# Kernel tuning notes

Hardware: AMD Instinct MI355X
Metric: run time of the kernel (lower is better)

Reference implementation:

```python
import jax, jax.numpy as jnp
import numpy as np

NUM_EXPERTS = 64
TOP_K = 8
HIDDEN = 2048
MLP = 768
TOKENS = 1024


def setup_inputs() -> dict:
    key = jax.random.key(0)
    ks = jax.random.split(key, 5)
    hidden_states = jax.random.normal(ks[0], (TOKENS, HIDDEN), dtype=jnp.float32)
    # lecun-normal-ish scaling (std = 1/sqrt(fan_in))
    router_w = jax.random.normal(ks[1], (HIDDEN, NUM_EXPERTS), dtype=jnp.float32) / np.sqrt(HIDDEN)
    gate_proj = jax.random.normal(ks[2], (NUM_EXPERTS, HIDDEN, MLP), dtype=jnp.float32) / np.sqrt(HIDDEN)
    up_proj = jax.random.normal(ks[3], (NUM_EXPERTS, HIDDEN, MLP), dtype=jnp.float32) / np.sqrt(HIDDEN)
    down_proj = jax.random.normal(ks[4], (NUM_EXPERTS, MLP, HIDDEN), dtype=jnp.float32) / np.sqrt(MLP)
    return {
        "hidden_states": hidden_states,
        "router_w": router_w,
        "gate_proj": gate_proj,
        "up_proj": up_proj,
        "down_proj": down_proj,
    }


def reference(hidden_states, router_w, gate_proj, up_proj, down_proj):
    # Router: [T, E]
    router_logits = hidden_states @ router_w
    # Top-k routing, softmax renormalized over the selected k (norm_topk_prob=True)
    routing_weights, selected_experts = jax.lax.top_k(router_logits, k=TOP_K)
    routing_weights = jax.nn.softmax(routing_weights, axis=-1)  # [T, k]

    sel_flat = selected_experts.ravel()  # [T*k] int32
    # Duplicate each token for each of its k experts: [T*k, H]
    x_exp = jnp.repeat(hidden_states, TOP_K, axis=0)

    # prepare_routing: sort token copies by expert id, count per-expert group sizes
    sort_idx = jnp.argsort(sel_flat)          # stable sort of expert ids
    x_sorted = x_exp[sort_idx]                # [T*k, H] grouped by expert
    group_sizes = jnp.zeros((NUM_EXPERTS,), dtype=jnp.int32).at[sel_flat].add(1)
    unsort_idx = jnp.argsort(sort_idx)

    # Grouped GEMMs (megablox-style) via ragged_dot
    gate_out = jax.lax.ragged_dot(x_sorted, gate_proj, group_sizes)   # [T*k, M]
    up_out = jax.lax.ragged_dot(x_sorted, up_proj, group_sizes)       # [T*k, M]
    down_out = jax.lax.ragged_dot(jax.nn.silu(gate_out) * up_out, down_proj, group_sizes)  # [T*k, H]

    # Unsort back to (token, k) order and combine with routing weights
    unsorted = down_out[unsort_idx].reshape(-1, TOP_K, HIDDEN)
    return jnp.sum(unsorted * routing_weights[..., None], axis=1)  # [T, H]
```

## Files before the change

### kernel.cpp

```cpp
#include <hip/hip_runtime.h>
#include <hip/hip_bf16.h>

#define T_TOKENS 1024
#define HID      2048
#define NEXP     64
#define TOPK     8
#define MLP      768
#define NPAIR    (T_TOKENS * TOPK)

typedef __bf16 bf16x8 __attribute__((ext_vector_type(8)));
typedef float  f32x4  __attribute__((ext_vector_type(4)));
typedef unsigned int u32x2 __attribute__((ext_vector_type(2)));
typedef unsigned int u32x4 __attribute__((ext_vector_type(4)));

#define LDK 40

static __device__ __forceinline__ unsigned short f2bf(float f) {
    __hip_bfloat16 h = __float2bfloat16(f);
    unsigned short u;
    __builtin_memcpy(&u, &h, sizeof(u));
    return u;
}
static __device__ __forceinline__ unsigned int pk2bf(float a, float b) {
    return (unsigned int)f2bf(a) | ((unsigned int)f2bf(b) << 16);
}

__global__ __launch_bounds__(256) void router_topk_kernel(
    const float* __restrict__ hs, const float* __restrict__ rw,
    int* __restrict__ sel, float* __restrict__ wts, unsigned short* __restrict__ xb)
{
    const int lane = threadIdx.x & 63;
    const int tg   = threadIdx.x >> 6;
    const int t    = blockIdx.x * 4 + tg;

    {
        const float* xr = hs + (size_t)t * HID;
        unsigned short* xw = xb + (size_t)t * HID;
        #pragma unroll
        for (int c = 0; c < 4; ++c) {
            int i = (lane + c * 64) * 8;
            f32x4 a = *(const f32x4*)(xr + i);
            f32x4 b = *(const f32x4*)(xr + i + 4);
            u32x4 v;
            v[0] = pk2bf(a[0], a[1]); v[1] = pk2bf(a[2], a[3]);
            v[2] = pk2bf(b[0], b[1]); v[3] = pk2bf(b[2], b[3]);
            *(u32x4*)(xw + i) = v;
        }
    }

    const float4* x4 = (const float4*)(hs + (size_t)t * HID);
    float acc = 0.f;
    for (int h4 = 0; h4 < HID / 4; ++h4) {
        float4 xv = x4[h4];
        int hb = h4 * 4 * NEXP + lane;
        acc += xv.x * rw[hb] + xv.y * rw[hb + NEXP]
             + xv.z * rw[hb + 2 * NEXP] + xv.w * rw[hb + 3 * NEXP];
    }

    float v = acc;
    float tv[TOPK]; int ti[TOPK];
    for (int i = 0; i < TOPK; ++i) {
        float m = v; int mi = lane;
        for (int off = 32; off > 0; off >>= 1) {
            float om  = __shfl_xor(m, off, 64);
            int   omi = __shfl_xor(mi, off, 64);
            if (om > m || (om == m && omi < mi)) { m = om; mi = omi; }
        }
        tv[i] = m; ti[i] = mi;
        if (lane == mi) v = -__builtin_inff();
    }
    if (lane == 0) {
        float mx = tv[0], s = 0.f, e[TOPK];
        for (int i = 0; i < TOPK; ++i) { e[i] = __expf(tv[i] - mx); s += e[i]; }
        float inv = 1.f / s;
        for (int i = 0; i < TOPK; ++i) {
            wts[t * TOPK + i] = e[i] * inv;
            sel[t * TOPK + i] = ti[i];
        }
    }
}

__global__ __launch_bounds__(1024) void route_kernel(
    const int* __restrict__ sel, int* __restrict__ offsets, int* __restrict__ rows)
{
    __shared__ int cnt[NEXP];
    __shared__ int cur[NEXP];
    const int t = threadIdx.x;
    if (t < NEXP) cnt[t] = 0;
    __syncthreads();
    int e[8];
    const int p0 = t * 8;
    #pragma unroll
    for (int j = 0; j < 8; ++j) {
        e[j] = sel[p0 + j];
        atomicAdd(&cnt[e[j]], 1);
    }
    __syncthreads();
    if (t == 0) {
        int s = 0;
        for (int i = 0; i < NEXP; ++i) { cur[i] = s; offsets[i] = s; s += cnt[i]; }
        offsets[NEXP] = s;
    }
    __syncthreads();
    #pragma unroll
    for (int j = 0; j < 8; ++j) {
        int pos = atomicAdd(&cur[e[j]], 1);
        rows[pos] = p0 + j;
    }
}

__global__ __launch_bounds__(512) void gateup_kernel(
    const unsigned short* __restrict__ xb, const float* __restrict__ gw,
    const float* __restrict__ uw, const int* __restrict__ offsets,
    const int* __restrict__ rows, unsigned short* __restrict__ hb)
{
    const int bid = blockIdx.x;
    const int sw  = (bid & 7) * 96 + (bid >> 3);
    const int e   = sw / 12;
    const int n0  = (sw % 12) * 64;

    const int r0 = offsets[e];
    const int nrows = offsets[e + 1] - r0;
    if (nrows <= 0) return;

    __shared__ __align__(16) float smemf[12800];
    unsigned short* smem = (unsigned short*)smemf;

    const int thr  = threadIdx.x;
    const int wave = thr >> 6;
    const int lane = thr & 63;
    const int wg   = wave & 3;
    const int isUp = wave >> 2;
    const int fr   = lane & 15;
    const int fq   = lane >> 4;

    const int ar = thr >> 3;
    const int ac = (thr & 7) * 4;

    const int wk2 = thr & 15;
    const int wnq = (thr & 255) >> 4;
    const float* wsrc = (thr >= 256 ? uw : gw)
        + (size_t)e * HID * MLP + (size_t)(2 * wk2) * MLP + n0 + wnq * 4;
    const int mofs = (thr >= 256) ? 10240 : 7680;

    const int NS = HID / 32;

    for (int m0 = 0; m0 < nrows; m0 += 192) {
        const unsigned short *ap0, *ap1, *ap2;
        bool av0, av1, av2;
        {
            int gr0 = m0 + ar, gr1 = m0 + ar + 64, gr2 = m0 + ar + 128;
            av0 = gr0 < nrows; av1 = gr1 < nrows; av2 = gr2 < nrows;
            int p0 = av0 ? rows[r0 + gr0] : 0;
            int p1 = av1 ? rows[r0 + gr1] : 0;
            int p2 = av2 ? rows[r0 + gr2] : 0;
            ap0 = xb + (size_t)(p0 >> 3) * HID + ac;
            ap1 = xb + (size_t)(p1 >> 3) * HID + ac;
            ap2 = xb + (size_t)(p2 >> 3) * HID + ac;
        }

        u32x2 va0, va1, va2;
        f32x4 w0e, w1e, w0o, w1o;
        const u32x2 z2 = (u32x2){0u, 0u};
        const f32x4 fz = (f32x4){0.f, 0.f, 0.f, 0.f};

        auto LOAD_A = [&](int s) {
            va0 = av0 ? *(const u32x2*)(ap0 + s * 32) : z2;
            va1 = av1 ? *(const u32x2*)(ap1 + s * 32) : z2;
            va2 = av2 ? *(const u32x2*)(ap2 + s * 32) : z2;
        };
        auto WRITE_A = [&](int s) {
            unsigned short* b = smem + (s & 1) * 12800;
            *(u32x2*)(b + ar * LDK + ac) = va0;
            *(u32x2*)(b + (ar + 64) * LDK + ac) = va1;
            *(u32x2*)(b + (ar + 128) * LDK + ac) = va2;
        };
        auto LOAD_WE = [&](int s) {
            const float* wp = wsrc + (size_t)s * 32 * MLP;
            w0e = *(const f32x4*)wp;  w1e = *(const f32x4*)(wp + MLP);
        };
        auto LOAD_WO = [&](int s) {
            const float* wp = wsrc + (size_t)s * 32 * MLP;
            w0o = *(const f32x4*)wp;  w1o = *(const f32x4*)(wp + MLP);
        };
        auto WRITE_WE = [&](int s) {
            unsigned short* wb = smem + (s & 1) * 12800 + mofs;
            #pragma unroll
            for (int i = 0; i < 4; ++i)
                *(unsigned int*)(wb + (wnq * 4 + i) * LDK + 2 * wk2) = pk2bf(w0e[i], w1e[i]);
        };
        auto WRITE_WO = [&](int s) {
            unsigned short* wb = smem + (s & 1) * 12800 + mofs;
            #pragma unroll
            for (int i = 0; i < 4; ++i)
                *(unsigned int*)(wb + (wnq * 4 + i) * LDK + 2 * wk2) = pk2bf(w0o[i], w1o[i]);
        };

        f32x4 acc[3][4];
        #pragma unroll
        for (int ms = 0; ms < 3; ++ms)
            #pragma unroll
            for (int ns = 0; ns < 4; ++ns) acc[ms][ns] = fz;

        const int rem = nrows - m0 - wg * 48;

        LOAD_WE(0);
        LOAD_WO(1);
        LOAD_A(0);
        WRITE_WE(0);
        WRITE_A(0);
        LOAD_A(1);
        asm volatile("s_waitcnt lgkmcnt(0)" ::: "memory");
        __builtin_amdgcn_s_barrier();

        #define GU_MFMA(BB)                                                          \
        {                                                                            \
            const unsigned short* wbb = (BB) + mofs;                                 \
            bf16x8 aF0, aF1, aF2, wF0, wF1, wF2, wF3;                                \
            wF0 = *(const bf16x8*)(wbb + (0 * 16 + fr) * LDK + fq * 8);              \
            wF1 = *(const bf16x8*)(wbb + (1 * 16 + fr) * LDK + fq * 8);              \
            wF2 = *(const bf16x8*)(wbb + (2 * 16 + fr) * LDK + fq * 8);              \
            wF3 = *(const bf16x8*)(wbb + (3 * 16 + fr) * LDK + fq * 8);              \
            aF0 = *(const bf16x8*)((BB) + (wg * 48 + fr) * LDK + fq * 8);            \
            aF1 = *(const bf16x8*)((BB) + (wg * 48 + 16 + fr) * LDK + fq * 8);       \
            aF2 = *(const bf16x8*)((BB) + (wg * 48 + 32 + fr) * LDK + fq * 8);       \
            if (rem > 0) {                                                           \
                acc[0][0] = __builtin_amdgcn_mfma_f32_16x16x32_bf16(aF0, wF0, acc[0][0], 0, 0, 0); \
                acc[0][1] = __builtin_amdgcn_mfma_f32_16x16x32_bf16(aF0, wF1, acc[0][1], 0, 0, 0); \
                acc[0][2] = __builtin_amdgcn_mfma_f32_16x16x32_bf16(aF0, wF2, acc[0][2], 0, 0, 0); \
                acc[0][3] = __builtin_amdgcn_mfma_f32_16x16x32_bf16(aF0, wF3, acc[0][3], 0, 0, 0); \
            }                                                                        \
            if (rem > 16) {                                                          \
                acc[1][0] = __builtin_amdgcn_mfma_f32_16x16x32_bf16(aF1, wF0, acc[1][0], 0, 0, 0); \
                acc[1][1] = __builtin_amdgcn_mfma_f32_16x16x32_bf16(aF1, wF1, acc[1][1], 0, 0, 0); \
                acc[1][2] = __builtin_amdgcn_mfma_f32_16x16x32_bf16(aF1, wF2, acc[1][2], 0, 0, 0); \
                acc[1][3] = __builtin_amdgcn_mfma_f32_16x16x32_bf16(aF1, wF3, acc[1][3], 0, 0, 0); \
            }                                                                        \
            if (rem > 32) {                                                          \
                acc[2][0] = __builtin_amdgcn_mfma_f32_16x16x32_bf16(aF2, wF0, acc[2][0], 0, 0, 0); \
                acc[2][1] = __builtin_amdgcn_mfma_f32_16x16x32_bf16(aF2, wF1, acc[2][1], 0, 0, 0); \
                acc[2][2] = __builtin_amdgcn_mfma_f32_16x16x32_bf16(aF2, wF2, acc[2][2], 0, 0, 0); \
                acc[2][3] = __builtin_amdgcn_mfma_f32_16x16x32_bf16(aF2, wF3, acc[2][3], 0, 0, 0); \
            }                                                                        \
        }

        for (int s = 0; s < NS; s += 2) {
            if (s + 2 < NS) LOAD_WE(s + 2);
            GU_MFMA(smem)
            WRITE_WO(s + 1);
            WRITE_A(s + 1);
            if (s + 2 < NS) LOAD_A(s + 2);
            asm volatile("s_waitcnt lgkmcnt(0)" ::: "memory");
            __builtin_amdgcn_s_barrier();
            if (s + 3 < NS) LOAD_WO(s + 3);
            GU_MFMA(smem + 12800)
            if (s + 2 < NS) { WRITE_WE(s + 2); WRITE_A(s + 2); }
            if (s + 3 < NS) LOAD_A(s + 3);
            asm volatile("s_waitcnt lgkmcnt(0)" ::: "memory");
            __builtin_amdgcn_s_barrier();
        }
        #undef GU_MFMA

        float* xbf = smemf;
        if (isUp) {
            #pragma unroll
            for (int ms = 0; ms < 3; ++ms)
                #pragma unroll
                for (int i = 0; i < 4; ++i) {
                    int lrow = wg * 48 + ms * 16 + fq * 4 + i;
                    #pragma unroll
                    for (int ns = 0; ns < 4; ++ns)
                        xbf[lrow * 65 + ns * 16 + fr] = acc[ms][ns][i];
                }
        }
        __syncthreads();
        if (!isUp) {
            #pragma unroll
            for (int ms = 0; ms < 3; ++ms)
                #pragma unroll
                for (int i = 0; i < 4; ++i) {
                    int lrow = wg * 48 + ms * 16 + fq * 4 + i;
                    int grow = m0 + lrow;
                    if (grow < nrows) {
                        unsigned short* drow = hb + (size_t)(r0 + grow) * MLP + n0;
                        #pragma unroll
                        for (int ns = 0; ns < 4; ++ns) {
                            float g = acc[ms][ns][i];
                            float u = xbf[lrow * 65 + ns * 16 + fr];
                            float h = g * u / (1.f + __expf(-g));
                            drow[ns * 16 + fr] = f2bf(h);
                        }
                    }
                }
        }
        __syncthreads();
    }
}

template <int USE_ATOMIC>
__global__ __launch_bounds__(256, 2) void down_kernel_t(
    const unsigned short* __restrict__ hb, const float* __restrict__ dw,
    const int* __restrict__ offsets, const int* __restrict__ rows,
    const float* __restrict__ wts, float* __restrict__ outp)
{
    const int bid = blockIdx.x;
    const int sw  = (bid & 7) * 128 + (bid >> 3);
    const int e   = sw >> 4;
    const int n0  = (sw & 15) * 128;

    const int r0 = offsets[e];
    const int nrows = offsets[e + 1] - r0;
    if (nrows <= 0) return;

    __shared__ __align__(16) float smemf[12800];
    unsigned short* smem = (unsigned short*)smemf;

    const int thr  = threadIdx.x;
    const int wave = thr >> 6;
    const int lane = thr & 63;
    const int wg   = wave & 1;
    const int wn   = wave >> 1;
    const int fr   = lane & 15;
    const int fq   = lane >> 4;

    const int ar = thr >> 2;
    const int ac = (thr & 3) * 8;

    const int wk2 = thr & 15;
    const int nst = (thr >> 4) * 8;
    const float* wsrc = dw + (size_t)e * MLP * HID + (size_t)(2 * wk2) * HID + n0 + nst;

    const int NS = MLP / 32;

    for (int m0 = 0; m0 < nrows; m0 += 192) {
        const bool av0 = (m0 + ar)       < nrows;
        const bool av1 = (m0 + ar + 64)  < nrows;
        const bool av2 = (m0 + ar + 128) < nrows;
        const unsigned short* hp0 = hb + (size_t)(r0 + m0 + ar) * MLP + ac;
        const unsigned short* hp1 = hp0 + (size_t)64  * MLP;
        const unsigned short* hp2 = hp0 + (size_t)128 * MLP;

        u32x4 ua0, ua1, ua2;
        f32x4 wAe, wBe, wCe, wDe, wAo, wBo, wCo, wDo;
        const u32x4 uz = (u32x4){0u, 0u, 0u, 0u};
        const f32x4 fz = (f32x4){0.f, 0.f, 0.f, 0.f};

        auto LOAD_A = [&](int s) {
            ua0 = av0 ? *(const u32x4*)(hp0 + s * 32) : uz;
            ua1 = av1 ? *(const u32x4*)(hp1 + s * 32) : uz;
            ua2 = av2 ? *(const u32x4*)(hp2 + s * 32) : uz;
        };
        auto WRITE_A = [&](int s) {
            unsigned short* b = smem + (s & 1) * 12800;
            *(u32x4*)(b + ar * LDK + ac) = ua0;
            *(u32x4*)(b + (ar + 64) * LDK + ac) = ua1;
            *(u32x4*)(b + (ar + 128) * LDK + ac) = ua2;
        };
        auto LOAD_WE = [&](int s) {
            const float* wp = wsrc + (size_t)s * 32 * HID;
            wAe = *(const f32x4*)wp;        wBe = *(const f32x4*)(wp + 4);
            wCe = *(const f32x4*)(wp + HID); wDe = *(const f32x4*)(wp + HID + 4);
        };
        auto LOAD_WO = [&](int s) {
            const float* wp = wsrc + (size_t)s * 32 * HID;
            wAo = *(const f32x4*)wp;        wBo = *(const f32x4*)(wp + 4);
            wCo = *(const f32x4*)(wp + HID); wDo = *(const f32x4*)(wp + HID + 4);
        };
        auto WRITE_WE = [&](int s) {
            unsigned short* wb = smem + (s & 1) * 12800 + 7680;
            #pragma unroll
            for (int j = 0; j < 4; ++j) {
                *(unsigned int*)(wb + (nst + j) * LDK + 2 * wk2)     = pk2bf(wAe[j], wCe[j]);
                *(unsigned int*)(wb + (nst + 4 + j) * LDK + 2 * wk2) = pk2bf(wBe[j], wDe[j]);
            }
        };
        auto WRITE_WO = [&](int s) {
            unsigned short* wb = smem + (s & 1) * 12800 + 7680;
            #pragma unroll
            for (int j = 0; j < 4; ++j) {
                *(unsigned int*)(wb + (nst + j) * LDK + 2 * wk2)     = pk2bf(wAo[j], wCo[j]);
                *(unsigned int*)(wb + (nst + 4 + j) * LDK + 2 * wk2) = pk2bf(wBo[j], wDo[j]);
            }
        };

        f32x4 acc[6][4];
        #pragma unroll
        for (int ms = 0; ms < 6; ++ms)
            #pragma unroll
            for (int ns = 0; ns < 4; ++ns) acc[ms][ns] = fz;

        const int rem = nrows - m0 - wg * 96;

        auto STEP = [&](const unsigned short* bb) {
            const unsigned short* wbb = bb + 7680;
            bf16x8 wF0 = *(const bf16x8*)(wbb + (wn * 64 + 0 * 16 + fr) * LDK + fq * 8);
            bf16x8 wF1 = *(const bf16x8*)(wbb + (wn * 64 + 1 * 16 + fr) * LDK + fq * 8);
            bf16x8 wF2 = *(const bf16x8*)(wbb + (wn * 64 + 2 * 16 + fr) * LDK + fq * 8);
            bf16x8 wF3 = *(const bf16x8*)(wbb + (wn * 64 + 3 * 16 + fr) * LDK + fq * 8);
            bf16x8 aF[6];
            #pragma unroll
            for (int ms = 0; ms < 6; ++ms)
                aF[ms] = *(const bf16x8*)(bb + (wg * 96 + ms * 16 + fr) * LDK + fq * 8);
            #pragma unroll
            for (int ms = 0; ms < 6; ++ms) {
                if (rem > ms * 16) {
                    acc[ms][0] = __builtin_amdgcn_mfma_f32_16x16x32_bf16(aF[ms], wF0, acc[ms][0], 0, 0, 0);
                    acc[ms][1] = __builtin_amdgcn_mfma_f32_16x16x32_bf16(aF[ms], wF1, acc[ms][1], 0, 0, 0);
                    acc[ms][2] = __builtin_amdgcn_mfma_f32_16x16x32_bf16(aF[ms], wF2, acc[ms][2], 0, 0, 0);
                    acc[ms][3] = __builtin_amdgcn_mfma_f32_16x16x32_bf16(aF[ms], wF3, acc[ms][3], 0, 0, 0);
                }
            }
        };

        LOAD_WE(0);
        LOAD_WO(1);
        LOAD_A(0);
        WRITE_WE(0);
        WRITE_A(0);
        LOAD_A(1);
        asm volatile("s_waitcnt lgkmcnt(0)" ::: "memory");
        __builtin_amdgcn_s_barrier();

        for (int s = 0; s < NS; s += 2) {
            if (s + 2 < NS) LOAD_WE(s + 2);
            STEP(smem);
            WRITE_WO(s + 1);
            WRITE_A(s + 1);
            if (s + 2 < NS) LOAD_A(s + 2);
            asm volatile("s_waitcnt lgkmcnt(0)" ::: "memory");
            __builtin_amdgcn_s_barrier();
            if (s + 3 < NS) LOAD_WO(s + 3);
            STEP(smem + 12800);
            if (s + 2 < NS) { WRITE_WE(s + 2); WRITE_A(s + 2); }
            if (s + 3 < NS) LOAD_A(s + 3);
            asm volatile("s_waitcnt lgkmcnt(0)" ::: "memory");
            __builtin_amdgcn_s_barrier();
        }

        #pragma unroll
        for (int ms = 0; ms < 6; ++ms) {
            #pragma unroll
            for (int i = 0; i < 4; ++i) {
                int lrow = wg * 96 + ms * 16 + fq * 4 + i;
                int grow = m0 + lrow;
                if (grow < nrows) {
                    int p = rows[r0 + grow];
                    if (USE_ATOMIC) {
                        float w = wts[p];
                        float* orow = outp + (size_t)(p >> 3) * HID + n0 + wn * 64;
                        #pragma unroll
                        for (int ns = 0; ns < 4; ++ns)
                            atomicAdd(orow + ns * 16 + fr, acc[ms][ns][i] * w);
                    } else {
                        float* orow = outp + (size_t)p * HID + n0 + wn * 64;
                        #pragma unroll
                        for (int ns = 0; ns < 4; ++ns)
                            orow[ns * 16 + fr] = acc[ms][ns][i];
                    }
                }
            }
        }
        __syncthreads();
    }
}

__global__ __launch_bounds__(256) void combine_kernel(
    const float* __restrict__ pout, const float* __restrict__ wts,
    float* __restrict__ out)
{
    const int idx = blockIdx.x * 256 + threadIdx.x;
    const int t   = idx >> 9;
    const int c4  = (idx & 511) * 4;

    const float* w8 = wts + t * TOPK;
    const float* pr = pout + (size_t)t * TOPK * HID + c4;
    f32x4 s = (f32x4){0.f, 0.f, 0.f, 0.f};
    #pragma unroll
    for (int j = 0; j < TOPK; ++j) {
        f32x4 v = *(const f32x4*)(pr + (size_t)j * HID);
        float w = w8[j];
        s[0] += w * v[0]; s[1] += w * v[1]; s[2] += w * v[2]; s[3] += w * v[3];
    }
    *(f32x4*)(out + (size_t)t * HID + c4) = s;
}

extern "C" void kernel_launch(void* const* d_in, const int* in_sizes, int n_in,
                              void* d_out, int out_size, void* d_ws, size_t ws_size,
                              hipStream_t stream)
{
    const float* hs = (const float*)d_in[0];
    const float* rw = (const float*)d_in[1];
    const float* gw = (const float*)d_in[2];
    const float* uw = (const float*)d_in[3];
    const float* dw = (const float*)d_in[4];
    float* out = (float*)d_out;

    char* ws = (char*)d_ws;
    int*   sel     = (int*)(ws);
    float* wts     = (float*)(ws + 32768);
    int*   offsets = (int*)(ws + 65792);
    int*   rows    = (int*)(ws + 66560);
    unsigned short* xb = (unsigned short*)(ws + 99328);
    unsigned short* hb = (unsigned short*)(ws + 99328 + 4194304);
    float* pout = (float*)(ws + 99328 + 4194304 + 12582912);
    const size_t need = 99328ull + 4194304 + 12582912 + (size_t)NPAIR * HID * 4;

    router_topk_kernel<<<T_TOKENS / 4, 256, 0, stream>>>(hs, rw, sel, wts, xb);
    route_kernel<<<1, 1024, 0, stream>>>(sel, offsets, rows);
    gateup_kernel<<<768, 512, 0, stream>>>(xb, gw, uw, offsets, rows, hb);

    if (ws_size >= need) {
        down_kernel_t<0><<<1024, 256, 0, stream>>>(hb, dw, offsets, rows, wts, pout);
        combine_kernel<<<T_TOKENS * HID / 4 / 256, 256, 0, stream>>>(pout, wts, out);
    } else {
        hipMemsetAsync(out, 0, (size_t)T_TOKENS * HID * sizeof(float), stream);
        down_kernel_t<1><<<1024, 256, 0, stream>>>(hb, dw, offsets, rows, wts, out);
    }
}
```

Measured before the change: 1.163 ms.

## Add 512-thread down-projection kernel with 8 waves and smaller per-wave tiles

```diff
diff --git a/kernel.cpp b/kernel.cpp
--- a/kernel.cpp
+++ b/kernel.cpp
@@ -297,11 +297,169 @@
     }
 }
 
-template <int USE_ATOMIC>
-__global__ __launch_bounds__(256, 2) void down_kernel_t(
+__global__ __launch_bounds__(512) void down2_kernel(
     const unsigned short* __restrict__ hb, const float* __restrict__ dw,
     const int* __restrict__ offsets, const int* __restrict__ rows,
-    const float* __restrict__ wts, float* __restrict__ outp)
+    float* __restrict__ pout)
+{
+    const int bid = blockIdx.x;
+    const int sw  = (bid & 7) * 128 + (bid >> 3);
+    const int e   = sw >> 4;
+    const int n0  = (sw & 15) * 128;
+
+    const int r0 = offsets[e];
+    const int nrows = offsets[e + 1] - r0;
+    if (nrows <= 0) return;
+
+    __shared__ __align__(16) unsigned short smem[2 * 12800];
+
+    const int thr  = threadIdx.x;
+    const int wave = thr >> 6;
+    const int lane = thr & 63;
+    const int wg   = wave & 3;
+    const int wc   = wave >> 2;
+    const int fr   = lane & 15;
+    const int fq   = lane >> 4;
+
+    const int ar0 = thr >> 2;
+    const int ac  = (thr & 3) * 8;
+    const int ar1 = 128 + (thr >> 2);
+    const bool hasS1 = thr < 256;
+
+    const int wk2 = thr & 15;
+    const int wnq = thr >> 4;
+    const float* wsrc = dw + (size_t)e * MLP * HID + (size_t)(2 * wk2) * HID + n0 + wnq * 4;
+
+    const int NS = MLP / 32;
+
+    for (int m0 = 0; m0 < nrows; m0 += 192) {
+        const bool av0 = (m0 + ar0) < nrows;
+        const bool av1 = hasS1 && (m0 + ar1) < nrows;
+        const unsigned short* hp0 = hb + (size_t)(r0 + m0 + ar0) * MLP + ac;
+        const unsigned short* hp1 = hb + (size_t)(r0 + m0 + ar1) * MLP + ac;
+
+        u32x4 ua0, ua1;
+        f32x4 w0e, w1e, w0o, w1o;
+        const u32x4 uz = (u32x4){0u, 0u, 0u, 0u};
+        const f32x4 fz = (f32x4){0.f, 0.f, 0.f, 0.f};
+
+        auto LOAD_A = [&](int s) {
+            ua0 = av0 ? *(const u32x4*)(hp0 + s * 32) : uz;
+            ua1 = av1 ? *(const u32x4*)(hp1 + s * 32) : uz;
+        };
+        auto WRITE_A = [&](int s) {
+            unsigned short* b = smem + (s & 1) * 12800;
+            *(u32x4*)(b + ar0 * LDK + ac) = ua0;
+            if (hasS1) *(u32x4*)(b + ar1 * LDK + ac) = ua1;
+        };
+        auto LOAD_WE = [&](int s) {
+            const float* wp = wsrc + (size_t)s * 32 * HID;
+            w0e = *(const f32x4*)wp;  w1e = *(const f32x4*)(wp + HID);
+        };
+        auto LOAD_WO = [&](int s) {
+            const float* wp = wsrc + (size_t)s * 32 * HID;
+            w0o = *(const f32x4*)wp;  w1o = *(const f32x4*)(wp + HID);
+        };
+        auto WRITE_WE = [&](int s) {
+            unsigned short* wb = smem + (s & 1) * 12800 + 7680;
+            #pragma unroll
+            for (int i = 0; i < 4; ++i)
+                *(unsigned int*)(wb + (wnq * 4 + i) * LDK + 2 * wk2) = pk2bf(w0e[i], w1e[i]);
+        };
+        auto WRITE_WO = [&](int s) {
+            unsigned short* wb = smem + (s & 1) * 12800 + 7680;
+            #pragma unroll
+            for (int i = 0; i < 4; ++i)
+                *(unsigned int*)(wb + (wnq * 4 + i) * LDK + 2 * wk2) = pk2bf(w0o[i], w1o[i]);
+        };
+
+        f32x4 acc[3][4];
+        #pragma unroll
+        for (int ms = 0; ms < 3; ++ms)
+            #pragma unroll
+            for (int ns = 0; ns < 4; ++ns) acc[ms][ns] = fz;
+
+        const int rem = nrows - m0 - wg * 48;
+
+        LOAD_WE(0);
+        LOAD_WO(1);
+        LOAD_A(0);
+        WRITE_WE(0);
+        WRITE_A(0);
+        LOAD_A(1);
+        asm volatile("s_waitcnt lgkmcnt(0)" ::: "memory");
+        __builtin_amdgcn_s_barrier();
+
+        #define DN_MFMA(BB)                                                          \
+        {                                                                            \
+            const unsigned short* wbb = (BB) + 7680;                                 \
+            bf16x8 aF0, aF1, aF2, wF0, wF1, wF2, wF3;                                \
+            wF0 = *(const bf16x8*)(wbb + (wc * 64 + 0 * 16 + fr) * LDK + fq * 8);    \
+            wF1 = *(const bf16x8*)(wbb + (wc * 64 + 1 * 16 + fr) * LDK + fq * 8);    \
+            wF2 = *(const bf16x8*)(wbb + (wc * 64 + 2 * 16 + fr) * LDK + fq * 8);    \
+            wF3 = *(const bf16x8*)(wbb + (wc * 64 + 3 * 16 + fr) * LDK + fq * 8);    \
+            aF0 = *(const bf16x8*)((BB) + (wg * 48 + fr) * LDK + fq * 8);            \
+            aF1 = *(const bf16x8*)((BB) + (wg * 48 + 16 + fr) * LDK + fq * 8);       \
+            aF2 = *(const bf16x8*)((BB) + (wg * 48 + 32 + fr) * LDK + fq * 8);       \
+            if (rem > 0) {                                                           \
+                acc[0][0] = __builtin_amdgcn_mfma_f32_16x16x32_bf16(aF0, wF0, acc[0][0], 0, 0, 0); \
+                acc[0][1] = __builtin_amdgcn_mfma_f32_16x16x32_bf16(aF0, wF1, acc[0][1], 0, 0, 0); \
+                acc[0][2] = __builtin_amdgcn_mfma_f32_16x16x32_bf16(aF0, wF2, acc[0][2], 0, 0, 0); \
+                acc[0][3] = __builtin_amdgcn_mfma_f32_16x16x32_bf16(aF0, wF3, acc[0][3], 0, 0, 0); \
+            }                                                                        \
+            if (rem > 16) {                                                          \
+                acc[1][0] = __builtin_amdgcn_mfma_f32_16x16x32_bf16(aF1, wF0, acc[1][0], 0, 0, 0); \
+                acc[1][1] = __builtin_amdgcn_mfma_f32_16x16x32_bf16(aF1, wF1, acc[1][1], 0, 0, 0); \
+                acc[1][2] = __builtin_amdgcn_mfma_f32_16x16x32_bf16(aF1, wF2, acc[1][2], 0, 0, 0); \
+                acc[1][3] = __builtin_amdgcn_mfma_f32_16x16x32_bf16(aF1, wF3, acc[1][3], 0, 0, 0); \
+            }                                                                        \
+            if (rem > 32) {                                                          \
+                acc[2][0] = __builtin_amdgcn_mfma_f32_16x16x32_bf16(aF2, wF0, acc[2][0], 0, 0, 0); \
+                acc[2][1] = __builtin_amdgcn_mfma_f32_16x16x32_bf16(aF2, wF1, acc[2][1], 0, 0, 0); \
+                acc[2][2] = __builtin_amdgcn_mfma_f32_16x16x32_bf16(aF2, wF2, acc[2][2], 0, 0, 0); \
+                acc[2][3] = __builtin_amdgcn_mfma_f32_16x16x32_bf16(aF2, wF3, acc[2][3], 0, 0, 0); \
+            }                                                                        \
+        }
+
+        for (int s = 0; s < NS; s += 2) {
+            if (s + 2 < NS) LOAD_WE(s + 2);
+            DN_MFMA(smem)
+            WRITE_WO(s + 1);
+            WRITE_A(s + 1);
+            if (s + 2 < NS) LOAD_A(s + 2);
+            asm volatile("s_waitcnt lgkmcnt(0)" ::: "memory");
+            __builtin_amdgcn_s_barrier();
+            if (s + 3 < NS) LOAD_WO(s + 3);
+            DN_MFMA(smem + 12800)
+            if (s + 2 < NS) { WRITE_WE(s + 2); WRITE_A(s + 2); }
+            if (s + 3 < NS) LOAD_A(s + 3);
+            asm volatile("s_waitcnt lgkmcnt(0)" ::: "memory");
+            __builtin_amdgcn_s_barrier();
+        }
+        #undef DN_MFMA
+
+        #pragma unroll
+        for (int ms = 0; ms < 3; ++ms) {
+            #pragma unroll
+            for (int i = 0; i < 4; ++i) {
+                int grow = m0 + wg * 48 + ms * 16 + fq * 4 + i;
+                if (grow < nrows) {
+                    int p = rows[r0 + grow];
+                    float* orow = pout + (size_t)p * HID + n0 + wc * 64;
+                    #pragma unroll
+                    for (int ns = 0; ns < 4; ++ns)
+                        orow[ns * 16 + fr] = acc[ms][ns][i];
+                }
+            }
+        }
+        __syncthreads();
+    }
+}
+
+__global__ __launch_bounds__(256, 2) void down_atomic_kernel(
+    const unsigned short* __restrict__ hb, const float* __restrict__ dw,
+    const int* __restrict__ offsets, const int* __restrict__ rows,
+    const float* __restrict__ wts, float* __restrict__ out)
 {
     const int bid = blockIdx.x;
     const int sw  = (bid & 7) * 128 + (bid >> 3);
@@ -445,18 +603,11 @@
                 int grow = m0 + lrow;
                 if (grow < nrows) {
                     int p = rows[r0 + grow];
-                    if (USE_ATOMIC) {
-                        float w = wts[p];
-                        float* orow = outp + (size_t)(p >> 3) * HID + n0 + wn * 64;
-                        #pragma unroll
-                        for (int ns = 0; ns < 4; ++ns)
-                            atomicAdd(orow + ns * 16 + fr, acc[ms][ns][i] * w);
-                    } else {
-                        float* orow = outp + (size_t)p * HID + n0 + wn * 64;
-                        #pragma unroll
-                        for (int ns = 0; ns < 4; ++ns)
-                            orow[ns * 16 + fr] = acc[ms][ns][i];
-                    }
+                    float w = wts[p];
+                    float* orow = out + (size_t)(p >> 3) * HID + n0 + wn * 64;
+                    #pragma unroll
+                    for (int ns = 0; ns < 4; ++ns)
+                        atomicAdd(orow + ns * 16 + fr, acc[ms][ns][i] * w);
                 }
             }
         }
@@ -510,10 +661,10 @@
     gateup_kernel<<<768, 512, 0, stream>>>(xb, gw, uw, offsets, rows, hb);
 
     if (ws_size >= need) {
-        down_kernel_t<0><<<1024, 256, 0, stream>>>(hb, dw, offsets, rows, wts, pout);
+        down2_kernel<<<1024, 512, 0, stream>>>(hb, dw, offsets, rows, pout);
         combine_kernel<<<T_TOKENS * HID / 4 / 256, 256, 0, stream>>>(pout, wts, out);
     } else {
         hipMemsetAsync(out, 0, (size_t)T_TOKENS * HID * sizeof(float), stream);
-        down_kernel_t<1><<<1024, 256, 0, stream>>>(hb, dw, offsets, rows, wts, out);
-    }
-}
+        down_atomic_kernel<<<1024, 256, 0, stream>>>(hb, dw, offsets, rows, wts, out);
+    }
+}
```

After: 1.179 ms. No clear change (+1.4%).
